# Performance work log

Hardware: AMD Instinct MI355X
Metric: run time of the kernel (lower is better)

The kernel has to match this reference:

```python
import jax, jax.numpy as jnp
import numpy as np

N_HEADS = 16
NEG_INF = -1e30


def apply_rope(x, cos, sin):
    # x: (B, T, H, D); cos/sin: (>=T, D//2)
    d = x.shape[-1]
    x1, x2 = x[..., : d // 2], x[..., d // 2 :]
    c = cos[: x.shape[1], :][None, :, None, :]  # (1, T, 1, D//2)
    s = sin[: x.shape[1], :][None, :, None, :]
    return jnp.concatenate([x1 * c - x2 * s, x2 * c + x1 * s], axis=-1)


def setup_inputs() -> dict:
    key = jax.random.key(0)
    k1, k2, k3, k4, k5 = jax.random.split(key, 5)
    B, T, D = 4, 2048, 2048
    hd = D // N_HEADS
    scale = 0.02
    return {
        "x": jax.random.normal(k1, (B, T, D), dtype=jnp.float32),
        "cos": jax.random.uniform(k2, (T, hd // 2), dtype=jnp.float32),
        "sin": jax.random.uniform(k3, (T, hd // 2), dtype=jnp.float32),
        "W_qkv": jax.random.normal(k4, (3 * D, D), dtype=jnp.float32) * scale,
        "W_out": jax.random.normal(k5, (D, D), dtype=jnp.float32) * scale,
    }


def reference(x, cos, sin, W_qkv, W_out):
    B, T, D = x.shape
    H = N_HEADS
    hd = D // H
    # fused QKV projection (torch Linear: y = x @ W.T)
    qkv = jnp.einsum("btd,ed->bte", x, W_qkv).reshape(B, T, 3, H, hd)
    q, k, v = qkv[:, :, 0], qkv[:, :, 1], qkv[:, :, 2]
    q = apply_rope(q, cos, sin)
    k = apply_rope(k, cos, sin)
    # causal SDPA, scale = 1/sqrt(head_dim)
    scores = jnp.einsum("bthd,bshd->bhts", q, k) / jnp.sqrt(jnp.asarray(hd, x.dtype))
    causal = jnp.tril(jnp.ones((T, T), dtype=bool))  # (T, T)
    scores = jnp.where(causal[None, None, :, :], scores, NEG_INF)
    attn = jax.nn.softmax(scores, axis=-1)
    out = jnp.einsum("bhts,bshd->bthd", attn, v).reshape(B, T, D)
    return jnp.einsum("btd,ed->bte", out, W_out)
```

## Files before the change

kernel.cpp:

```cpp
#include <hip/hip_runtime.h>
#include <hip/hip_bf16.h>
#include <stdint.h>

#define TDIM 2048
#define DDIM 2048
#define BDIM 4
#define HDIM 16
#define HD   128
#define E3   6144
#define KDIM 2048

typedef unsigned short u16;
typedef __bf16 bf16x8 __attribute__((ext_vector_type(8)));
typedef float  f32x4  __attribute__((ext_vector_type(4)));

__device__ __forceinline__ u16 f2bf(float f) {
  union { float f; uint32_t u; } x; x.f = f;
  uint32_t r = x.u + 0x7fffu + ((x.u >> 16) & 1u);
  return (u16)(r >> 16);
}
__device__ __forceinline__ float bf2f(u16 u) {
  union { uint32_t u; float f; } x; x.u = ((uint32_t)u) << 16;
  return x.f;
}

__device__ __forceinline__ void load16(const void* g, void* l) {
  __builtin_amdgcn_global_load_lds(
      (const __attribute__((address_space(1))) void*)g,
      (__attribute__((address_space(3))) void*)l, 16, 0, 0);
}

__global__ void cvt_kernel(const float* __restrict__ in, u16* __restrict__ out, int n) {
  int i = (blockIdx.x * 256 + threadIdx.x) * 4;
  if (i >= n) return;
  float4 v = *(const float4*)(in + i);
  ushort4 o;
  o.x = f2bf(v.x); o.y = f2bf(v.y); o.z = f2bf(v.z); o.w = f2bf(v.w);
  *(ushort4*)(out + i) = o;
}

template <int MODE>
__global__ __launch_bounds__(256) void gemm_bt(
    const u16* __restrict__ A, const u16* __restrict__ Bm,
    u16* __restrict__ qkOut, u16* __restrict__ vtOut, float* __restrict__ fOut) {
  __shared__ __align__(16) u16 As[128 * 32];
  __shared__ __align__(16) u16 Bs[128 * 32];
  const int tid = threadIdx.x;
  const int bn = blockIdx.x, bm = blockIdx.y;
  const int w = tid >> 6, lane = tid & 63;
  const int wr = w >> 1, wc = w & 1;
  const int lrow = lane & 15, lgrp = lane >> 4;

  f32x4 acc[4][4];
#pragma unroll
  for (int m = 0; m < 4; ++m)
#pragma unroll
    for (int n = 0; n < 4; ++n) {
      acc[m][n][0] = 0.f; acc[m][n][1] = 0.f; acc[m][n][2] = 0.f; acc[m][n][3] = 0.f;
    }

  const size_t aRow = (size_t)bm * 128;
  const size_t bRow = (size_t)bn * 128;

  for (int kt = 0; kt < KDIM / 32; ++kt) {
    const int kb = kt * 32;
#pragma unroll
    for (int is = 0; is < 2; ++is) {
      int u = is * 256 + tid;
      int r = u >> 2, c = u & 3;
      load16(A + (aRow + r) * KDIM + kb + c * 8, (char*)As + (size_t)u * 16);
    }
#pragma unroll
    for (int is = 0; is < 2; ++is) {
      int u = is * 256 + tid;
      int r = u >> 2, c = u & 3;
      load16(Bm + (bRow + r) * KDIM + kb + c * 8, (char*)Bs + (size_t)u * 16);
    }
    __syncthreads();

    bf16x8 af[4], bfr[4];
#pragma unroll
    for (int m = 0; m < 4; ++m)
      af[m] = *(const bf16x8*)(As + (wr * 64 + m * 16 + lrow) * 32 + lgrp * 8);
#pragma unroll
    for (int n = 0; n < 4; ++n)
      bfr[n] = *(const bf16x8*)(Bs + (wc * 64 + n * 16 + lrow) * 32 + lgrp * 8);
#pragma unroll
    for (int m = 0; m < 4; ++m)
#pragma unroll
      for (int n = 0; n < 4; ++n)
        acc[m][n] = __builtin_amdgcn_mfma_f32_16x16x32_bf16(af[m], bfr[n], acc[m][n], 0, 0, 0);
    __syncthreads();
  }

  const int col_base = bn * 128 + wc * 64;
  const int row_base = bm * 128 + wr * 64;
#pragma unroll
  for (int m = 0; m < 4; ++m) {
    int row0 = row_base + m * 16 + lgrp * 4;
#pragma unroll
    for (int n = 0; n < 4; ++n) {
      int col = col_base + n * 16 + lrow;
      if (MODE == 0) {
        if (bn < 32) {
#pragma unroll
          for (int i = 0; i < 4; ++i)
            qkOut[(size_t)(row0 + i) * 4096 + col] = f2bf(acc[m][n][i]);
        } else {
          int e = col - 4096;
          int hh = e >> 7, d = e & 127;
          int bb = row0 >> 11, t0 = row0 & 2047;
          ushort4 pk;
          pk.x = f2bf(acc[m][n][0]); pk.y = f2bf(acc[m][n][1]);
          pk.z = f2bf(acc[m][n][2]); pk.w = f2bf(acc[m][n][3]);
          *(ushort4*)(vtOut + ((size_t)(bb * HDIM + hh) * HD + d) * TDIM + t0) = pk;
        }
      } else {
#pragma unroll
        for (int i = 0; i < 4; ++i)
          fOut[(size_t)(row0 + i) * DDIM + col] = acc[m][n][i];
      }
    }
  }
}

__global__ void rope_kernel(u16* __restrict__ qkbuf,
                            const float* __restrict__ cosb, const float* __restrict__ sinb) {
  int gid = blockIdx.x * 256 + threadIdx.x;
  int d4 = gid & 15;
  int h = (gid >> 4) & 15;
  int which = (gid >> 8) & 1;
  int row = gid >> 9;
  int t = row & 2047;
  u16* base = qkbuf + (size_t)row * 4096 + which * 2048 + h * HD + d4 * 4;
  ushort4 u1 = *(ushort4*)base;
  ushort4 u2 = *(ushort4*)(base + 64);
  float4 c = *(const float4*)(cosb + (size_t)t * 64 + d4 * 4);
  float4 s = *(const float4*)(sinb + (size_t)t * 64 + d4 * 4);
  float x1[4] = {bf2f(u1.x), bf2f(u1.y), bf2f(u1.z), bf2f(u1.w)};
  float x2[4] = {bf2f(u2.x), bf2f(u2.y), bf2f(u2.z), bf2f(u2.w)};
  float cc[4] = {c.x, c.y, c.z, c.w};
  float ss[4] = {s.x, s.y, s.z, s.w};
  ushort4 o1, o2;
  o1.x = f2bf(x1[0]*cc[0] - x2[0]*ss[0]); o2.x = f2bf(x2[0]*cc[0] + x1[0]*ss[0]);
  o1.y = f2bf(x1[1]*cc[1] - x2[1]*ss[1]); o2.y = f2bf(x2[1]*cc[1] + x1[1]*ss[1]);
  o1.z = f2bf(x1[2]*cc[2] - x2[2]*ss[2]); o2.z = f2bf(x2[2]*cc[2] + x1[2]*ss[2]);
  o1.w = f2bf(x1[3]*cc[3] - x2[3]*ss[3]); o2.w = f2bf(x2[3]*cc[3] + x1[3]*ss[3]);
  *(ushort4*)base = o1;
  *(ushort4*)(base + 64) = o2;
}

__global__ __launch_bounds__(256) void attn_kernel(const u16* __restrict__ qkbuf,
                                                   const u16* __restrict__ vtbuf,
                                                   u16* __restrict__ ao) {
  __shared__ __align__(16) u16 Ks[64 * 128];
  __shared__ __align__(16) u16 Vs[128 * 64];
  __shared__ __align__(16) u16 Ps[4][16 * 64];
  const int tid = threadIdx.x;
  const int w = tid >> 6, lane = tid & 63;
  const int lrow = lane & 15, lgrp = lane >> 4;
  const int bh = blockIdx.y, b = bh >> 4, h = bh & 15;

  const u16* qbase = qkbuf + (size_t)b * TDIM * 4096 + h * HD;
  const u16* kbase = qbase + 2048;
  const u16* vbase = vtbuf + (size_t)(b * HDIM + h) * HD * TDIM;

  const float scale2 = 0.08838834764831845f * 1.4426950408889634f;

  for (int pass = 0; pass < 2; ++pass) {
    const int qt = pass == 0 ? (int)blockIdx.x : (31 - (int)blockIdx.x);
    const int q0 = qt * 64;

    const int qrow = q0 + w * 16 + lrow;
    bf16x8 qf[4];
#pragma unroll
    for (int kb = 0; kb < 4; ++kb)
      qf[kb] = *(const bf16x8*)(qbase + (size_t)qrow * 4096 + kb * 32 + lgrp * 8);

    f32x4 po[8];
#pragma unroll
    for (int n = 0; n < 8; ++n) { po[n][0]=0.f; po[n][1]=0.f; po[n][2]=0.f; po[n][3]=0.f; }
    float m_i[4], l_i[4];
#pragma unroll
    for (int i = 0; i < 4; ++i) { m_i[i] = -1e30f; l_i[i] = 0.f; }

    const int ntiles = qt + 1;
    for (int it = 0; it < ntiles; ++it) {
      const int kv0 = it * 64;
      __syncthreads();
#pragma unroll
      for (int is = 0; is < 4; ++is) {
        int u = is * 256 + tid;
        int r = u >> 4, blk = u & 15;
        load16(kbase + (size_t)(kv0 + r) * 4096 + ((blk ^ (r & 7)) * 8),
               (char*)Ks + (size_t)u * 16);
      }
#pragma unroll
      for (int is = 0; is < 4; ++is) {
        int u = is * 256 + tid;
        int r = u >> 3, blk = u & 7;
        load16(vbase + (size_t)r * TDIM + kv0 + ((blk ^ (r & 7)) * 8),
               (char*)Vs + (size_t)u * 16);
      }
      __syncthreads();

      f32x4 sacc[4];
#pragma unroll
      for (int c = 0; c < 4; ++c) {
        sacc[c][0]=0.f; sacc[c][1]=0.f; sacc[c][2]=0.f; sacc[c][3]=0.f;
        int row = c * 16 + lrow;
        int swz = row & 7;
#pragma unroll
        for (int kb = 0; kb < 4; ++kb) {
          bf16x8 kf = *(const bf16x8*)(Ks + row * 128 + ((kb * 4 + lgrp) ^ swz) * 8);
          sacc[c] = __builtin_amdgcn_mfma_f32_16x16x32_bf16(qf[kb], kf, sacc[c], 0, 0, 0);
        }
      }

      float sv[4][4];
      float mt[4] = {-1e30f, -1e30f, -1e30f, -1e30f};
#pragma unroll
      for (int c = 0; c < 4; ++c) {
        int kg = kv0 + c * 16 + lrow;
#pragma unroll
        for (int i = 0; i < 4; ++i) {
          int qg = q0 + w * 16 + lgrp * 4 + i;
          float v = sacc[c][i] * scale2;
          if (kg > qg) v = -1e30f;
          sv[c][i] = v;
          mt[i] = fmaxf(mt[i], v);
        }
      }
#pragma unroll
      for (int msk = 1; msk < 16; msk <<= 1)
#pragma unroll
        for (int i = 0; i < 4; ++i) mt[i] = fmaxf(mt[i], __shfl_xor(mt[i], msk));

      bool grow = (mt[0] > m_i[0] + 11.f) || (mt[1] > m_i[1] + 11.f) ||
                  (mt[2] > m_i[2] + 11.f) || (mt[3] > m_i[3] + 11.f);
      if (__any(grow)) {
#pragma unroll
        for (int i = 0; i < 4; ++i) {
          float mn = fmaxf(m_i[i], mt[i]);
          float corr = exp2f(m_i[i] - mn);
          m_i[i] = mn;
          l_i[i] *= corr;
#pragma unroll
          for (int n = 0; n < 8; ++n) po[n][i] *= corr;
        }
      }

      float ps[4] = {0.f, 0.f, 0.f, 0.f};
      float pv[4][4];
#pragma unroll
      for (int c = 0; c < 4; ++c)
#pragma unroll
        for (int i = 0; i < 4; ++i) {
          float p = exp2f(sv[c][i] - m_i[i]);
          pv[c][i] = p;
          ps[i] += p;
        }
#pragma unroll
      for (int msk = 1; msk < 16; msk <<= 1)
#pragma unroll
        for (int i = 0; i < 4; ++i) ps[i] += __shfl_xor(ps[i], msk);
#pragma unroll
      for (int i = 0; i < 4; ++i) l_i[i] += ps[i];

#pragma unroll
      for (int c = 0; c < 4; ++c) {
        int kcol = c * 16 + lrow;
#pragma unroll
        for (int i = 0; i < 4; ++i) {
          int prow = lgrp * 4 + i;
          Ps[w][prow * 64 + (((kcol >> 3) ^ (prow & 7)) * 8) + (kcol & 7)] = f2bf(pv[c][i]);
        }
      }
      bf16x8 pa[2];
#pragma unroll
      for (int kk = 0; kk < 2; ++kk)
        pa[kk] = *(const bf16x8*)(&Ps[w][lrow * 64 + (((kk * 4 + lgrp) ^ (lrow & 7)) * 8)]);
#pragma unroll
      for (int n = 0; n < 8; ++n) {
        int row = n * 16 + lrow;
        int swz = row & 7;
#pragma unroll
        for (int kk = 0; kk < 2; ++kk) {
          bf16x8 vf = *(const bf16x8*)(Vs + row * 64 + (((kk * 4 + lgrp) ^ swz) * 8));
          po[n] = __builtin_amdgcn_mfma_f32_16x16x32_bf16(pa[kk], vf, po[n], 0, 0, 0);
        }
      }
    }

#pragma unroll
    for (int n = 0; n < 8; ++n)
#pragma unroll
      for (int i = 0; i < 4; ++i) {
        int qg = q0 + w * 16 + lgrp * 4 + i;
        float v = po[n][i] / l_i[i];
        ao[(size_t)(b * TDIM + qg) * DDIM + h * HD + n * 16 + lrow] = f2bf(v);
      }
  }
}

extern "C" void kernel_launch(void* const* d_in, const int* in_sizes, int n_in,
                              void* d_out, int out_size, void* d_ws, size_t ws_size,
                              hipStream_t stream) {
  const float* x    = (const float*)d_in[0];
  const float* cosb = (const float*)d_in[1];
  const float* sinb = (const float*)d_in[2];
  const float* wqkv = (const float*)d_in[3];
  const float* wout = (const float*)d_in[4];
  float* out = (float*)d_out;
  char* ws = (char*)d_ws;
  u16* xb  = (u16*)(ws);
  u16* wqb = (u16*)(ws + 33554432);
  u16* wob = (u16*)(ws + 58720256);
  u16* qkb = (u16*)(ws + 67108864);
  u16* vtb = (u16*)(ws + 134217728);

  cvt_kernel<<<16384, 256, 0, stream>>>(x, xb, 16777216);
  cvt_kernel<<<12288, 256, 0, stream>>>(wqkv, wqb, 12582912);
  cvt_kernel<<<4096, 256, 0, stream>>>(wob ? wout : wout, wob, 4194304);
  gemm_bt<0><<<dim3(48, 64), 256, 0, stream>>>(xb, wqb, qkb, vtb, nullptr);
  rope_kernel<<<16384, 256, 0, stream>>>(qkb, cosb, sinb);
  attn_kernel<<<dim3(16, 64), 256, 0, stream>>>(qkb, vtb, xb);
  gemm_bt<1><<<dim3(16, 64), 256, 0, stream>>>(xb, wob, nullptr, nullptr, out);
}
```

Baseline: 734.0 us.

## Double GEMM K-tile with swizzled LDS; skip mask off-diagonal; defer row-sum reduction

The GEMM now loads a 64-wide K slice per iteration into XOR-swizzled shared memory and runs two MFMA sub-steps per barrier pair. This halves the number of syncs and is meant to reduce LDS bank conflicts. In attention, the causal mask is applied only on the diagonal tile. The per-tile softmax row-sum shuffle reduction becomes per-lane accumulation with a single cross-lane reduction at the end. Together these cut barrier, masking and shuffle overhead, at the cost of more shared memory per GEMM block.

```diff
diff --git a/kernel.cpp b/kernel.cpp
--- a/kernel.cpp
+++ b/kernel.cpp
@@ -43,8 +43,8 @@
 __global__ __launch_bounds__(256) void gemm_bt(
     const u16* __restrict__ A, const u16* __restrict__ Bm,
     u16* __restrict__ qkOut, u16* __restrict__ vtOut, float* __restrict__ fOut) {
-  __shared__ __align__(16) u16 As[128 * 32];
-  __shared__ __align__(16) u16 Bs[128 * 32];
+  __shared__ __align__(16) u16 As[128 * 64];
+  __shared__ __align__(16) u16 Bs[128 * 64];
   const int tid = threadIdx.x;
   const int bn = blockIdx.x, bm = blockIdx.y;
   const int w = tid >> 6, lane = tid & 63;
@@ -62,34 +62,43 @@
   const size_t aRow = (size_t)bm * 128;
   const size_t bRow = (size_t)bn * 128;
 
-  for (int kt = 0; kt < KDIM / 32; ++kt) {
-    const int kb = kt * 32;
-#pragma unroll
-    for (int is = 0; is < 2; ++is) {
+  for (int kt = 0; kt < KDIM / 64; ++kt) {
+    const int kb = kt * 64;
+#pragma unroll
+    for (int is = 0; is < 4; ++is) {
       int u = is * 256 + tid;
-      int r = u >> 2, c = u & 3;
-      load16(A + (aRow + r) * KDIM + kb + c * 8, (char*)As + (size_t)u * 16);
-    }
-#pragma unroll
-    for (int is = 0; is < 2; ++is) {
+      int r = u >> 3, blk = u & 7;
+      load16(A + (aRow + r) * KDIM + kb + ((blk ^ (r & 7)) * 8),
+             (char*)As + (size_t)u * 16);
+    }
+#pragma unroll
+    for (int is = 0; is < 4; ++is) {
       int u = is * 256 + tid;
-      int r = u >> 2, c = u & 3;
-      load16(Bm + (bRow + r) * KDIM + kb + c * 8, (char*)Bs + (size_t)u * 16);
+      int r = u >> 3, blk = u & 7;
+      load16(Bm + (bRow + r) * KDIM + kb + ((blk ^ (r & 7)) * 8),
+             (char*)Bs + (size_t)u * 16);
     }
     __syncthreads();
 
-    bf16x8 af[4], bfr[4];
-#pragma unroll
-    for (int m = 0; m < 4; ++m)
-      af[m] = *(const bf16x8*)(As + (wr * 64 + m * 16 + lrow) * 32 + lgrp * 8);
-#pragma unroll
-    for (int n = 0; n < 4; ++n)
-      bfr[n] = *(const bf16x8*)(Bs + (wc * 64 + n * 16 + lrow) * 32 + lgrp * 8);
-#pragma unroll
-    for (int m = 0; m < 4; ++m)
-#pragma unroll
-      for (int n = 0; n < 4; ++n)
-        acc[m][n] = __builtin_amdgcn_mfma_f32_16x16x32_bf16(af[m], bfr[n], acc[m][n], 0, 0, 0);
+#pragma unroll
+    for (int kk = 0; kk < 2; ++kk) {
+      bf16x8 af[4], bfr[4];
+#pragma unroll
+      for (int m = 0; m < 4; ++m) {
+        int row = wr * 64 + m * 16 + lrow;
+        af[m] = *(const bf16x8*)(As + row * 64 + (((kk * 4 + lgrp) ^ (row & 7)) * 8));
+      }
+#pragma unroll
+      for (int n = 0; n < 4; ++n) {
+        int row = wc * 64 + n * 16 + lrow;
+        bfr[n] = *(const bf16x8*)(Bs + row * 64 + (((kk * 4 + lgrp) ^ (row & 7)) * 8));
+      }
+#pragma unroll
+      for (int m = 0; m < 4; ++m)
+#pragma unroll
+        for (int n = 0; n < 4; ++n)
+          acc[m][n] = __builtin_amdgcn_mfma_f32_16x16x32_bf16(af[m], bfr[n], acc[m][n], 0, 0, 0);
+    }
     __syncthreads();
   }
 
@@ -219,17 +228,28 @@
 
       float sv[4][4];
       float mt[4] = {-1e30f, -1e30f, -1e30f, -1e30f};
-#pragma unroll
-      for (int c = 0; c < 4; ++c) {
-        int kg = kv0 + c * 16 + lrow;
-#pragma unroll
-        for (int i = 0; i < 4; ++i) {
-          int qg = q0 + w * 16 + lgrp * 4 + i;
-          float v = sacc[c][i] * scale2;
-          if (kg > qg) v = -1e30f;
-          sv[c][i] = v;
-          mt[i] = fmaxf(mt[i], v);
-        }
+      if (it == qt) {
+#pragma unroll
+        for (int c = 0; c < 4; ++c) {
+          int kg = kv0 + c * 16 + lrow;
+#pragma unroll
+          for (int i = 0; i < 4; ++i) {
+            int qg = q0 + w * 16 + lgrp * 4 + i;
+            float v = sacc[c][i] * scale2;
+            if (kg > qg) v = -1e30f;
+            sv[c][i] = v;
+            mt[i] = fmaxf(mt[i], v);
+          }
+        }
+      } else {
+#pragma unroll
+        for (int c = 0; c < 4; ++c)
+#pragma unroll
+          for (int i = 0; i < 4; ++i) {
+            float v = sacc[c][i] * scale2;
+            sv[c][i] = v;
+            mt[i] = fmaxf(mt[i], v);
+          }
       }
 #pragma unroll
       for (int msk = 1; msk < 16; msk <<= 1)
@@ -250,7 +270,6 @@
         }
       }
 
-      float ps[4] = {0.f, 0.f, 0.f, 0.f};
       float pv[4][4];
 #pragma unroll
       for (int c = 0; c < 4; ++c)
@@ -258,14 +277,8 @@
         for (int i = 0; i < 4; ++i) {
           float p = exp2f(sv[c][i] - m_i[i]);
           pv[c][i] = p;
-          ps[i] += p;
-        }
-#pragma unroll
-      for (int msk = 1; msk < 16; msk <<= 1)
-#pragma unroll
-        for (int i = 0; i < 4; ++i) ps[i] += __shfl_xor(ps[i], msk);
-#pragma unroll
-      for (int i = 0; i < 4; ++i) l_i[i] += ps[i];
+          l_i[i] += p;
+        }
 
 #pragma unroll
       for (int c = 0; c < 4; ++c) {
@@ -292,6 +305,10 @@
       }
     }
 
+#pragma unroll
+    for (int msk = 1; msk < 16; msk <<= 1)
+#pragma unroll
+      for (int i = 0; i < 4; ++i) l_i[i] += __shfl_xor(l_i[i], msk);
 #pragma unroll
     for (int n = 0; n < 8; ++n)
 #pragma unroll
@@ -321,7 +338,7 @@
 
   cvt_kernel<<<16384, 256, 0, stream>>>(x, xb, 16777216);
   cvt_kernel<<<12288, 256, 0, stream>>>(wqkv, wqb, 12582912);
-  cvt_kernel<<<4096, 256, 0, stream>>>(wob ? wout : wout, wob, 4194304);
+  cvt_kernel<<<4096, 256, 0, stream>>>(wout, wob, 4194304);
   gemm_bt<0><<<dim3(48, 64), 256, 0, stream>>>(xb, wqb, qkb, vtb, nullptr);
   rope_kernel<<<16384, 256, 0, stream>>>(qkb, cosb, sinb);
   attn_kernel<<<dim3(16, 64), 256, 0, stream>>>(qkb, vtb, xb);
```

Measured after the change: 664.3 us. 1.1x faster.
